# Kernel optimization log

Measured on AMD Instinct MI355X. Metric: run time of the kernel, lower is better.

## Reference

```python
import jax, jax.numpy as jnp
import numpy as np

B, C, D, H, W = 4, 1, 192, 192, 192
SMALL = 4            # int(192 * bias_scale=0.025)
BIAS_STD = 0.7
MAX_SIGMA = 3.0
TRUNCATE = 4.0
K = 2 * int(TRUNCATE * MAX_SIGMA) + 1   # fixed truncated kernel size = 25
N_LABELS = 32
TABLE = 128          # static remap-table size (>= max source label, >= max dest)


def setup_inputs() -> dict:
    key = jax.random.key(0)
    k1, k2, k3, k4, k5 = jax.random.split(key, 5)
    return {
        "x": jax.random.normal(k1, (B, C, D, H, W), jnp.float32),
        "small_bias": jax.random.normal(k2, (B, 1, SMALL, SMALL, SMALL), jnp.float32),
        "sigma01": jax.random.uniform(k3, (B, 3), jnp.float32),
        "labels": jax.random.randint(k4, (B, 1, D, H, W), 0, N_LABELS, jnp.int32),
        "source_values": jnp.arange(N_LABELS, dtype=jnp.int64),
        "dest_values": jax.random.randint(k5, (N_LABELS,), 0, 100, jnp.int64),
    }


def _lin_weights(n_in, n_out):
    """Dense 1D linear-interp matrix [n_out, n_in], align_corners=True."""
    pos = jnp.linspace(0.0, n_in - 1.0, n_out)
    i0 = jnp.clip(jnp.floor(pos).astype(jnp.int32), 0, n_in - 2)
    f = pos - i0.astype(pos.dtype)
    r = jnp.arange(n_out)
    Wm = jnp.zeros((n_out, n_in), jnp.float32)
    Wm = Wm.at[r, i0].add(1.0 - f).at[r, i0 + 1].add(f)
    return Wm


def _bias_field(small_bias):
    # trilinear align_corners upsample [B,1,s,s,s] -> [B,1,D,H,W], separable
    b = small_bias * BIAS_STD
    b = jnp.einsum('bcxyz,dx->bcdyz', b, _lin_weights(SMALL, D))
    b = jnp.einsum('bcdyz,hy->bcdhz', b, _lin_weights(SMALL, H))
    b = jnp.einsum('bcdhz,wz->bcdhw', b, _lin_weights(SMALL, W))
    return b


def _gauss_kernels(sigma):
    """sigma [3] -> normalized kernels [3, K]; identity (delta) where sigma<0.01."""
    ar = jnp.arange(K, dtype=jnp.float32) - K // 2
    s = jnp.maximum(sigma, 1e-3)[:, None]
    g = jnp.exp(-0.5 * (ar[None, :] ** 2) / (s ** 2))
    g = g / g.sum(-1, keepdims=True)
    delta = jnp.zeros((K,), jnp.float32).at[K // 2].set(1.0)
    return jnp.where(sigma[:, None] >= 0.01, g, delta[None, :])


def _blur_axis(x, k, axis):
    # x [C,D,H,W]; depthwise 1D conv along `axis` with replicate (edge) padding
    p = K // 2
    xm = jnp.moveaxis(x, axis, -1)
    shp = xm.shape
    xm = xm.reshape(-1, 1, shp[-1])
    xm = jnp.pad(xm, ((0, 0), (0, 0), (p, p)), mode='edge')
    out = jax.lax.conv_general_dilated(xm, k.reshape(1, 1, K), (1,), 'VALID')
    return jnp.moveaxis(out.reshape(shp), -1, axis)


def _blur_sample(x, kernels):
    # x [C,D,H,W], kernels [3,K]; separable blur over D,H,W
    for i, ax in enumerate((1, 2, 3)):
        x = _blur_axis(x, kernels[i], ax)
    return x


def reference(x, small_bias, sigma01, labels, source_values, dest_values):
    # 1) bias-field corruption: x * exp(upsampled random field)
    img = x * jnp.exp(_bias_field(small_bias))
    # 2) dynamic per-sample Gaussian blur, sigma in [0, MAX_SIGMA]
    kernels = jax.vmap(_gauss_kernels)(sigma01 * MAX_SIGMA)   # [B,3,K]
    img = jax.vmap(_blur_sample)(img, kernels)
    # 3) label remap via lookup table gather
    mapping = jnp.zeros((TABLE,), jnp.int32).at[source_values].set(
        dest_values.astype(jnp.int32))
    labels_out = mapping[labels]
    return img, labels_out
```

## Files before the change

kernel.cpp:

```cpp
#include <hip/hip_runtime.h>
#include <hip/hip_fp16.h>
#include <cstdint>
#include <cstddef>

#define Bc 4
#define Dd 192
#define Hh 192
#define Ww 192
#define KK 25
#define RR 12
#define VOL (Bc*Dd*Hh*Ww)
#define SP 216
#define SPU (SP/2)
#define SH 98
#define RIN 56
#define RD  56

typedef unsigned short u16;
typedef unsigned int   u32;
typedef __fp16 h2 __attribute__((ext_vector_type(2)));
typedef __fp16 h8 __attribute__((ext_vector_type(8)));
typedef float  f32x4 __attribute__((ext_vector_type(4)));

__device__ inline u32 pk2(float a, float b) {
    return __builtin_bit_cast(u32, __builtin_amdgcn_cvt_pkrtz(a, b));
}

__global__ void setup_tables_kernel(const float* __restrict__ sigma01,
                                    const int* __restrict__ src,
                                    const int* __restrict__ dst,
                                    u32* __restrict__ kern2,
                                    int* __restrict__ mapping,
                                    float* __restrict__ mapf) {
    int t = threadIdx.x;
    if (t < 128) mapping[t] = 0;
    __syncthreads();
    if (t < 32) {
        int s = src[t];
        if (s >= 0 && s < 128) mapping[s] = dst[t];
    }
    __syncthreads();
    if (t < 128) mapf[t] = (float)mapping[t];
    if (t < Bc * 3) {
        float sig = sigma01[t] * 3.0f;
        float s = fmaxf(sig, 1e-3f);
        float g[KK];
        float sum = 0.0f;
        #pragma unroll
        for (int i = 0; i < KK; i++) {
            float a = (float)(i - RR);
            float v = expf(-0.5f * a * a / (s * s));
            g[i] = v; sum += v;
        }
        float inv = 1.0f / sum;
        #pragma unroll
        for (int i = 0; i < KK; i++) {
            float v = g[i] * inv;
            if (sig < 0.01f) v = (i == RR) ? 1.0f : 0.0f;
            u16 hb = __builtin_bit_cast(u16, __float2half(v));
            kern2[t * KK + i] = (u32)hb | ((u32)hb << 16);
        }
    }
}

__global__ __launch_bounds__(256) void pass_wh_remap_kernel(
    const float* __restrict__ x, u16* __restrict__ outB,
    const u32* __restrict__ kern2, const float* __restrict__ sb,
    const int4* __restrict__ labels, float4* __restrict__ lab_out,
    const float* __restrict__ mapf) {
    __shared__ u16 P[RIN * SP];
    __shared__ float2 ch2[RIN * 3];
    __shared__ u16 kpadW[64];
    const int tid = threadIdx.x;
    const int hx = blockIdx.x;
    const int d  = blockIdx.y;
    const int b  = blockIdx.z;

    if (tid < RIN) {
        int r = tid;
        int hrow = min(max(32 * hx - RR + r, 0), Hh - 1);
        float pos_d = d * (3.0f / 191.0f);
        int   id0   = min((int)pos_d, 2);
        float fd    = pos_d - (float)id0;
        float pos_h = hrow * (3.0f / 191.0f);
        int   ih0   = min((int)pos_h, 2);
        float fh    = pos_h - (float)ih0;
        const float* sbA = sb + b * 64 + id0 * 16 + ih0 * 4;
        float c[4];
        #pragma unroll
        for (int k = 0; k < 4; k++) {
            float v00 = sbA[k],      v01 = sbA[4 + k];
            float v10 = sbA[16 + k], v11 = sbA[20 + k];
            float vd0 = (1.f - fd) * v00 + fd * v10;
            float vd1 = (1.f - fd) * v01 + fd * v11;
            c[k] = ((1.f - fh) * vd0 + fh * vd1) * 0.7f;
        }
        #pragma unroll
        for (int k = 0; k < 3; k++)
            ch2[r * 3 + k] = make_float2(c[k], c[k + 1] - c[k]);
    }
    if (tid >= 64 && tid < 128) {
        int i = tid - 64;
        int t = i - 15;
        u16 v = (t >= 0 && t < KK) ? (u16)(kern2[(b * 3 + 2) * KK + t] & 0xFFFFu)
                                   : (u16)0;
        kpadW[i] = v;
    }
    __syncthreads();

    const size_t pbase = ((size_t)b * Dd + d) * (size_t)(Hh * Ww);
    #pragma unroll
    for (int it = 0; it < 11; it++) {
        int i4 = it * 256 + tid;
        if (i4 < RIN * 48) {
            int r = i4 / 48, w4 = i4 % 48;
            int w = 4 * w4;
            int hrow = min(max(32 * hx - RR + r, 0), Hh - 1);
            float4 v = *(const float4*)(x + pbase + (size_t)hrow * Ww + w);
            float rs[4];
            #pragma unroll
            for (int j = 0; j < 4; j++) {
                float pw = (float)(w + j) * (3.0f / 191.0f);
                int sel = (pw >= 1.0f) + (pw >= 2.0f);
                float2 cd = ch2[r * 3 + sel];
                float bias = fmaf(pw - (float)sel, cd.y, cd.x);
                float val = (j == 0 ? v.x : j == 1 ? v.y : j == 2 ? v.z : v.w);
                rs[j] = val * __expf(bias);
            }
            u32* dstp = (u32*)&P[r * SP + RR + w];
            dstp[0] = pk2(rs[0], rs[1]);
            dstp[1] = pk2(rs[2], rs[3]);
            if (w4 == 0) {
                u32 hh = pk2(rs[0], rs[0]);
                u32* hp = (u32*)&P[r * SP];
                #pragma unroll
                for (int m = 0; m < 6; m++) hp[m] = hh;
            } else if (w4 == 47) {
                u32 hh = pk2(rs[3], rs[3]);
                u32* hp = (u32*)&P[r * SP + RR + Ww];
                #pragma unroll
                for (int m = 0; m < 6; m++) hp[m] = hh;
            }
        }
    }
    __syncthreads();

    {
        const int bid = (b * Dd + d) * 6 + hx;
        const int4* lp = labels + (size_t)bid * 1536 + tid;
        int4 lab[6];
        #pragma unroll
        for (int m = 0; m < 6; m++) lab[m] = lp[m * 256];
        float4* op = lab_out + (size_t)bid * 1536 + tid;
        #pragma unroll
        for (int m = 0; m < 6; m++) {
            int4 l = lab[m];
            float4 o;
            o.x = mapf[min(max(l.x, 0), 127)];
            o.y = mapf[min(max(l.y, 0), 127)];
            o.z = mapf[min(max(l.z, 0), 127)];
            o.w = mapf[min(max(l.w, 0), 127)];
            op[m * 256] = o;
        }
    }

    {
        const int ln = tid & 63, wv = tid >> 6;
        const int c  = ln & 15;
        const int kg = ln >> 4;
        h8 B0, B1;
        #pragma unroll
        for (int j = 0; j < 8; j++) {
            int k = kg * 8 + j;
            B0[j] = __builtin_bit_cast(__fp16, kpadW[15 + k - c]);
            int i1 = 15 + k + 32 - c;
            B1[j] = __builtin_bit_cast(__fp16, (i1 < 64) ? kpadW[i1] : (u16)0);
        }
        const int ra = min(wv * 16 + c, RIN - 1);
        const u16* rowp = &P[ra * SP + kg * 8];
        const int rd0 = wv * 16 + kg * 4;
        h8 F[10];
        #pragma unroll
        for (int f = 0; f < 10; f++)
            F[f] = __builtin_bit_cast(h8, *(const uint4*)(rowp + f * 16));
        #pragma unroll
        for (int ct = 0; ct < 8; ct++) {
            f32x4 acc = {0.f, 0.f, 0.f, 0.f};
            acc = __builtin_amdgcn_mfma_f32_16x16x32_f16(F[ct], B0, acc, 0, 0, 0);
            acc = __builtin_amdgcn_mfma_f32_16x16x32_f16(F[ct + 2], B1, acc, 0, 0, 0);
            #pragma unroll
            for (int m = 0; m < 4; m++) {
                int rd = rd0 + m;
                if (rd < RIN)
                    P[rd * SP + RR + ct * 16 + c] =
                        __builtin_bit_cast(u16, (__fp16)acc[m]);
            }
        }
        h8 G[4];
        G[0] = __builtin_bit_cast(h8, *(const uint4*)(rowp + 160));
        G[1] = __builtin_bit_cast(h8, *(const uint4*)(rowp + 176));
        G[2] = __builtin_bit_cast(h8, *(const uint4*)(rowp + ((kg == 0) ? 192 : 160)));
        G[3] = __builtin_bit_cast(h8, *(const uint4*)(rowp + ((kg == 0) ? 208 : 160)));
        #pragma unroll
        for (int ct = 8; ct < 12; ct++) {
            h8 A0 = (ct < 10) ? F[ct] : G[ct - 10];
            h8 A1 = G[ct - 8];
            f32x4 acc = {0.f, 0.f, 0.f, 0.f};
            acc = __builtin_amdgcn_mfma_f32_16x16x32_f16(A0, B0, acc, 0, 0, 0);
            acc = __builtin_amdgcn_mfma_f32_16x16x32_f16(A1, B1, acc, 0, 0, 0);
            #pragma unroll
            for (int m = 0; m < 4; m++) {
                int rd = rd0 + m;
                if (rd < RIN)
                    P[rd * SP + RR + ct * 16 + c] =
                        __builtin_bit_cast(u16, (__fp16)acc[m]);
            }
        }
    }
    __syncthreads();

    {
        const u32* kh2 = kern2 + (b * 3 + 1) * KK;
        u32* outp = (u32*)(outB + pbase);
        #pragma unroll
        for (int it = 0; it < 3; it++) {
            int item = it * 256 + tid;
            int col = item % 96;
            int g = item / 96;
            u32 win[28];
            #pragma unroll
            for (int i = 0; i < 28; i++)
                win[i] = *((const u32*)P + (g * 4 + i) * SPU + 6 + col);
            h2 acc[4];
            #pragma unroll
            for (int j = 0; j < 4; j++) acc[j] = (h2)(0.0f);
            #pragma unroll
            for (int t = 0; t < KK; t++) {
                h2 kv = __builtin_bit_cast(h2, kh2[t]);
                #pragma unroll
                for (int j = 0; j < 4; j++)
                    acc[j] += kv * __builtin_bit_cast(h2, win[j + t]);
            }
            #pragma unroll
            for (int j = 0; j < 4; j++)
                outp[(32 * hx + g * 4 + j) * 96 + col] =
                    __builtin_bit_cast(u32, acc[j]);
        }
    }
}

__global__ __launch_bounds__(192) void pass_d_kernel(
    const u16* __restrict__ in, float* __restrict__ img,
    const u32* __restrict__ kern2) {
    __shared__ __attribute__((aligned(16))) u16 T[RD * SH];
    const int tid = threadIdx.x;
    const int w0 = blockIdx.x * 96;
    const int d0 = blockIdx.y * 32;
    const int z = blockIdx.z;
    const int h = z % Hh, b = z / Hh;
    const u32* kp = kern2 + b * 3 * KK;
    #pragma unroll
    for (int k = 0; k < 4; k++) {
        int idx = k * 192 + tid;
        if (idx < RD * 12) {
            int r = idx / 12, sg = idx % 12;
            int dd = min(max(d0 + r - RR, 0), Dd - 1);
            uint4 v = *(const uint4*)(in + (((size_t)b * Dd + dd) * Hh + h) * (size_t)Ww + w0 + sg * 8);
            u32* p = (u32*)&T[r * SH + sg * 8];
            p[0] = v.x; p[1] = v.y; p[2] = v.z; p[3] = v.w;
        }
    }
    __syncthreads();
    const int p = tid % 48;
    const int g = tid / 48;
    const int ob = g * 8;
    u32 win[32];
    #pragma unroll
    for (int i = 0; i < 32; i++) win[i] = *(const u32*)&T[(ob + i) * SH + 2 * p];
    h2 acc[8];
    #pragma unroll
    for (int j = 0; j < 8; j++) acc[j] = (h2)(0.0f);
    #pragma unroll
    for (int t = 0; t < KK; t++) {
        h2 kv = __builtin_bit_cast(h2, kp[t]);
        #pragma unroll
        for (int j = 0; j < 8; j++)
            acc[j] += kv * __builtin_bit_cast(h2, win[j + t]);
    }
    #pragma unroll
    for (int j = 0; j < 8; j++) {
        h2 a = acc[j];
        float2 f = make_float2((float)a.x, (float)a.y);
        *(float2*)(img + (((size_t)b * Dd + (d0 + ob + j)) * Hh + h) * (size_t)Ww + w0 + 2 * p) = f;
    }
}

extern "C" void kernel_launch(void* const* d_in, const int* in_sizes, int n_in,
                              void* d_out, int out_size, void* d_ws, size_t ws_size,
                              hipStream_t stream) {
    const float* x          = (const float*)d_in[0];
    const float* small_bias = (const float*)d_in[1];
    const float* sigma01    = (const float*)d_in[2];
    const int*   labels     = (const int*)d_in[3];
    const int*   src        = (const int*)d_in[4];
    const int*   dst        = (const int*)d_in[5];

    float* out     = (float*)d_out;
    float* img     = out;
    float* lab_out = out + (size_t)VOL;

    u32*   kern2   = (u32*)((float*)d_ws + 384);
    int*   mapping = (int*)((float*)d_ws + 768);
    float* mapf    = (float*)d_ws + 896;
    u16*   Bb      = (u16*)((char*)d_ws + 8192);

    setup_tables_kernel<<<1, 128, 0, stream>>>(sigma01, src, dst, kern2,
                                               mapping, mapf);

    pass_wh_remap_kernel<<<dim3(6, Dd, Bc), 256, 0, stream>>>(
        x, Bb, kern2, small_bias,
        (const int4*)labels, (float4*)lab_out, mapf);
    pass_d_kernel<<<dim3(Ww / 96, Dd / 32, Bc * Hh), 192, 0, stream>>>(Bb, img, kern2);
}
```

Measured before the change: 134.3 us.

## Swizzle block indices across XCDs and split label remap between both passes

Both kernels now use a flattened 1D grid and remap block IDs so that consecutive logical tiles land on the same XCD (8-way swizzle), aiming for better L2 locality of overlapping halo reads. The label remap work is split: the W/H pass handles the first half of the volume and the D pass handles the second half. This balances memory traffic between the two kernels and hides the label loads behind the D-pass convolution. The risks are the added index arithmetic and some uncoalescing from the swizzle.

```diff
diff --git a/kernel.cpp b/kernel.cpp
--- a/kernel.cpp
+++ b/kernel.cpp
@@ -15,6 +15,7 @@
 #define SH 98
 #define RIN 56
 #define RD  56
+#define NXCD 8
 
 typedef unsigned short u16;
 typedef unsigned int   u32;
@@ -72,9 +73,12 @@
     __shared__ float2 ch2[RIN * 3];
     __shared__ u16 kpadW[64];
     const int tid = threadIdx.x;
-    const int hx = blockIdx.x;
-    const int d  = blockIdx.y;
-    const int b  = blockIdx.z;
+    const int swz = blockIdx.x;
+    const int orig = (swz & (NXCD - 1)) * 576 + (swz >> 3);
+    const int hx = orig % 6;
+    const int pd = orig / 6;
+    const int d  = pd % Dd;
+    const int b  = pd / Dd;
 
     if (tid < RIN) {
         int r = tid;
@@ -146,14 +150,13 @@
     __syncthreads();
 
     {
-        const int bid = (b * Dd + d) * 6 + hx;
-        const int4* lp = labels + (size_t)bid * 1536 + tid;
-        int4 lab[6];
-        #pragma unroll
-        for (int m = 0; m < 6; m++) lab[m] = lp[m * 256];
-        float4* op = lab_out + (size_t)bid * 1536 + tid;
-        #pragma unroll
-        for (int m = 0; m < 6; m++) {
+        const int4* lp = labels + (size_t)orig * 768 + tid;
+        int4 lab[3];
+        #pragma unroll
+        for (int m = 0; m < 3; m++) lab[m] = lp[m * 256];
+        float4* op = lab_out + (size_t)orig * 768 + tid;
+        #pragma unroll
+        for (int m = 0; m < 3; m++) {
             int4 l = lab[m];
             float4 o;
             o.x = mapf[min(max(l.x, 0), 127)];
@@ -249,14 +252,18 @@
     }
 }
 
-__global__ __launch_bounds__(192) void pass_d_kernel(
+__global__ __launch_bounds__(192) void pass_d_remap_kernel(
     const u16* __restrict__ in, float* __restrict__ img,
-    const u32* __restrict__ kern2) {
+    const u32* __restrict__ kern2,
+    const int4* __restrict__ labels, float4* __restrict__ lab_out,
+    const float* __restrict__ mapf) {
     __shared__ __attribute__((aligned(16))) u16 T[RD * SH];
     const int tid = threadIdx.x;
-    const int w0 = blockIdx.x * 96;
-    const int d0 = blockIdx.y * 32;
-    const int z = blockIdx.z;
+    const int swz = blockIdx.x;
+    const int orig = (swz & (NXCD - 1)) * 1152 + (swz >> 3);
+    const int w0 = (orig % 2) * 96;
+    const int d0 = ((orig / 2) % 6) * 32;
+    const int z  = orig / 12;
     const int h = z % Hh, b = z / Hh;
     const u32* kp = kern2 + b * 3 * KK;
     #pragma unroll
@@ -270,6 +277,9 @@
             p[0] = v.x; p[1] = v.y; p[2] = v.z; p[3] = v.w;
         }
     }
+    const size_t lbase = (size_t)(VOL / 8) + (size_t)orig * 384 + tid;
+    int4 la0 = labels[lbase];
+    int4 la1 = labels[lbase + 192];
     __syncthreads();
     const int p = tid % 48;
     const int g = tid / 48;
@@ -292,6 +302,19 @@
         h2 a = acc[j];
         float2 f = make_float2((float)a.x, (float)a.y);
         *(float2*)(img + (((size_t)b * Dd + (d0 + ob + j)) * Hh + h) * (size_t)Ww + w0 + 2 * p) = f;
+    }
+    {
+        float4 o0, o1;
+        o0.x = mapf[min(max(la0.x, 0), 127)];
+        o0.y = mapf[min(max(la0.y, 0), 127)];
+        o0.z = mapf[min(max(la0.z, 0), 127)];
+        o0.w = mapf[min(max(la0.w, 0), 127)];
+        o1.x = mapf[min(max(la1.x, 0), 127)];
+        o1.y = mapf[min(max(la1.y, 0), 127)];
+        o1.z = mapf[min(max(la1.z, 0), 127)];
+        o1.w = mapf[min(max(la1.w, 0), 127)];
+        lab_out[lbase] = o0;
+        lab_out[lbase + 192] = o1;
     }
 }
 
@@ -317,8 +340,9 @@
     setup_tables_kernel<<<1, 128, 0, stream>>>(sigma01, src, dst, kern2,
                                                mapping, mapf);
 
-    pass_wh_remap_kernel<<<dim3(6, Dd, Bc), 256, 0, stream>>>(
+    pass_wh_remap_kernel<<<4608, 256, 0, stream>>>(
         x, Bb, kern2, small_bias,
         (const int4*)labels, (float4*)lab_out, mapf);
-    pass_d_kernel<<<dim3(Ww / 96, Dd / 32, Bc * Hh), 192, 0, stream>>>(Bb, img, kern2);
-}
+    pass_d_remap_kernel<<<9216, 192, 0, stream>>>(
+        Bb, img, kern2, (const int4*)labels, (float4*)lab_out, mapf);
+}
```

After: 135.2 us. Within noise of the previous version (+0.7%).
